# Kernel optimization log

Measured on AMD Instinct MI355X. Metric: run time of the kernel, lower is better.

## Reference

```python
import jax, jax.numpy as jnp
import numpy as np

B, S, D, H, HD = 4, 2048, 1024, 16, 64


def setup_inputs() -> dict:
    key = jax.random.key(0)
    k1, k2, k3 = jax.random.split(key, 3)
    x = jax.random.normal(k1, (B, S, D), dtype=jnp.float32)
    w_attn = jax.random.normal(k2, (D, 3, H, HD), dtype=jnp.float32) * 0.02
    b_attn = jnp.zeros((3, H, HD), dtype=jnp.float32)
    w_proj = jax.random.normal(k3, (H, HD, D), dtype=jnp.float32) * 0.02
    b_proj = jnp.zeros((D,), dtype=jnp.float32)
    return {"x": x, "w_attn": w_attn, "b_attn": b_attn, "w_proj": w_proj, "b_proj": b_proj}


def reference(x, w_attn, b_attn, w_proj, b_proj):
    # c_attn: [B,S,D] x [D,3,H,HD] -> [B,3,H,S,HD]
    qkv = jnp.einsum('bsd,dqhe->bqhse', x, w_attn) + b_attn[None, :, :, None, :]
    q, k, v = qkv[:, 0], qkv[:, 1], qkv[:, 2]  # each [B,H,S,HD]
    scale = 1.0 / jnp.sqrt(jnp.asarray(HD, dtype=q.dtype))
    scores = jnp.einsum('bhse,bhte->bhst', q * scale, k)  # [B,H,S,S]
    causal = jnp.tril(jnp.ones((S, S), dtype=bool))
    scores = jnp.where(causal, scores, jnp.asarray(-1e9, dtype=scores.dtype))
    attn = jax.nn.softmax(scores, axis=-1)
    out = jnp.einsum('bhst,bhte->bhse', attn, v)  # [B,H,S,HD]
    # c_proj: contract (heads, head_size) -> embed
    return jnp.einsum('bhse,hed->bsd', out, w_proj) + b_proj
```

## Files before the change

kernel.cpp:

```cpp
#include <hip/hip_runtime.h>

#define NB 4
#define NS 2048
#define ND 1024
#define NH 16
#define NE 64
#define NM (NB*NS)

typedef __attribute__((ext_vector_type(8))) __bf16 bf16x8;
typedef __attribute__((ext_vector_type(8))) unsigned short us8;
typedef __attribute__((ext_vector_type(4))) float f32x4;

__device__ __forceinline__ float bf2f(unsigned short h) {
  union { unsigned u; float f; } c; c.u = ((unsigned)h) << 16; return c.f;
}
__device__ __forceinline__ unsigned short f2bf(float f) {
  union { float f; unsigned u; } c; c.f = f;
  return (unsigned short)((c.u + 0x7fffu + ((c.u >> 16) & 1u)) >> 16);
}
__device__ __forceinline__ void load16_to_lds(const void* g, void* l) {
  __builtin_amdgcn_global_load_lds(
      (__attribute__((address_space(1))) void*)(void*)(unsigned long long)(const char*)g,
      (__attribute__((address_space(3))) void*)l, 16, 0, 0);
}

__global__ void detect_dtype(const unsigned* __restrict__ x, int* __restrict__ flag) {
  __shared__ int cnt;
  if (threadIdx.x == 0) cnt = 0;
  __syncthreads();
  unsigned w = x[((unsigned)threadIdx.x * 16381u) & ((1u << 21) - 1u)];
  unsigned lo = w & 0xFFFFu;
  int e = (int)((lo >> 7) & 0xFF);
  int plausible = (lo == 0u) || (e >= 100 && e <= 142);
  atomicAdd(&cnt, plausible);
  __syncthreads();
  if (threadIdx.x == 0) *flag = (cnt >= 192) ? 1 : 0;
}

__global__ void conv_to_bf16(const void* __restrict__ src, unsigned short* __restrict__ dst,
                             int n, const int* __restrict__ flag) {
  int stride = gridDim.x * blockDim.x;
  int i0 = blockIdx.x * blockDim.x + threadIdx.x;
  if (*flag) {
    const unsigned short* s = (const unsigned short*)src;
    for (int i = i0; i < n; i += stride) dst[i] = s[i];
  } else {
    const float* s = (const float*)src;
    for (int i = i0; i < n; i += stride) dst[i] = f2bf(s[i]);
  }
}

__global__ __launch_bounds__(256) void transpose_conv(const void* __restrict__ in,
                                                      unsigned short* __restrict__ out,
                                                      int K, int N, const int* __restrict__ flag) {
  __shared__ unsigned short tile[32][33];
  int n0 = blockIdx.x * 32, k0 = blockIdx.y * 32;
  int tx = threadIdx.x, ty = threadIdx.y;
  if (*flag) {
    const unsigned short* p = (const unsigned short*)in;
#pragma unroll
    for (int i = 0; i < 4; ++i)
      tile[ty + 8*i][tx] = p[(size_t)(k0 + ty + 8*i) * N + n0 + tx];
  } else {
    const float* p = (const float*)in;
#pragma unroll
    for (int i = 0; i < 4; ++i)
      tile[ty + 8*i][tx] = f2bf(p[(size_t)(k0 + ty + 8*i) * N + n0 + tx]);
  }
  __syncthreads();
#pragma unroll
  for (int i = 0; i < 4; ++i)
    out[(size_t)(n0 + ty + 8*i) * K + k0 + tx] = tile[tx][ty + 8*i];
}

__device__ __forceinline__ void gemm_core(const unsigned short* __restrict__ A,
                                          const unsigned short* __restrict__ Bt,
                                          int K, int m0, int n0,
                                          unsigned short* As, unsigned short* Bs,
                                          f32x4 (&acc)[4][4]) {
  int t = threadIdx.x;
  int lane = t & 63;
  int w = t >> 6, wr = w >> 1, wc = w & 1;
  int frm = lane & 15, fko = (lane >> 4) * 8;
  for (int kk = 0; kk < K; kk += 32) {
#pragma unroll
    for (int c = 0; c < 2; ++c) {
      int L = c * 256 + t;
      int r = L >> 2, ko = (L & 3) * 8;
      load16_to_lds(A  + (size_t)(m0 + r) * K + kk + ko, (char*)As + L * 16);
      load16_to_lds(Bt + (size_t)(n0 + r) * K + kk + ko, (char*)Bs + L * 16);
    }
    __syncthreads();
    bf16x8 a[4], b[4];
#pragma unroll
    for (int i = 0; i < 4; ++i) a[i] = *(const bf16x8*)(As + (64*wr + 16*i + frm) * 32 + fko);
#pragma unroll
    for (int j = 0; j < 4; ++j) b[j] = *(const bf16x8*)(Bs + (64*wc + 16*j + frm) * 32 + fko);
#pragma unroll
    for (int i = 0; i < 4; ++i)
#pragma unroll
      for (int j = 0; j < 4; ++j)
        acc[i][j] = __builtin_amdgcn_mfma_f32_16x16x32_bf16(a[i], b[j], acc[i][j], 0, 0, 0);
    __syncthreads();
  }
}

__global__ __launch_bounds__(256) void gemm_qkv(const unsigned short* __restrict__ X,
                                                const unsigned short* __restrict__ W1T,
                                                const unsigned short* __restrict__ battn,
                                                unsigned short* __restrict__ qb,
                                                unsigned short* __restrict__ kb,
                                                unsigned short* __restrict__ vb) {
  __shared__ unsigned short As[128 * 32];
  __shared__ unsigned short Bs[128 * 32];
  int m0 = blockIdx.y * 128, n0 = blockIdx.x * 128;
  f32x4 acc[4][4] = {};
  gemm_core(X, W1T, ND, m0, n0, As, Bs, acc);
  int t = threadIdx.x, lane = t & 63, w = t >> 6, wr = w >> 1, wc = w & 1;
  int coln = lane & 15, rbase = (lane >> 4) * 4;
#pragma unroll
  for (int j = 0; j < 4; ++j) {
    int nn = n0 + 64*wc + 16*j + coln;
    int qq = nn >> 10;
    int h  = (nn >> 6) & 15;
    int e  = nn & 63;
    float bias = bf2f(battn[nn]);
    unsigned short* dst = (qq == 0) ? qb : ((qq == 1) ? kb : vb);
    float scale = (qq == 0) ? (0.125f * 1.44269504f) : 1.0f;
#pragma unroll
    for (int i = 0; i < 4; ++i) {
#pragma unroll
      for (int rr = 0; rr < 4; ++rr) {
        int mm = m0 + 64*wr + 16*i + rbase + rr;
        int bb = mm >> 11, s = mm & 2047;
        float v = (acc[i][j][rr] + bias) * scale;
        size_t idx;
        if (qq == 2) idx = (((size_t)bb * NH + h) * NE + e) * NS + s;
        else         idx = (((size_t)bb * NH + h) * NS + s) * NE + e;
        dst[idx] = f2bf(v);
      }
    }
  }
}

__global__ __launch_bounds__(256) void attn_causal(const unsigned short* __restrict__ qb,
                                                   const unsigned short* __restrict__ kb,
                                                   const unsigned short* __restrict__ vtb,
                                                   unsigned short* __restrict__ ob) {
  __shared__ unsigned short QPs[128 * 64];
  __shared__ unsigned short Ks[2][64 * 64];
  __shared__ unsigned short Vt[2][64 * 64];

  int t = threadIdx.x, lane = t & 63, w = t >> 6;
  int qd = lane >> 4, li = lane & 15;
  int sw0 = ((qd ^ (li & 7)) * 8);
  int sw1 = (((4 + qd) ^ (li & 7)) * 8);
  int p = blockIdx.x;
  int bh = blockIdx.y;
  size_t base = (size_t)bh * NS * NE;
  int bb = bh >> 4, hh = bh & 15;

  bf16x8 onesf;
#pragma unroll
  for (int j = 0; j < 8; ++j) onesf[j] = (__bf16)1.0f;

  auto stage_kv = [&](int k0, unsigned short* Ksb, unsigned short* Vtb) {
#pragma unroll
    for (int c = 0; c < 2; ++c) {
      int ch = c * 256 + t;
      int r = ch >> 3, jl = (ch & 7) ^ (r & 7);
      load16_to_lds(kb  + base + (size_t)(k0 + r) * NE + jl * 8, (char*)Ksb + ch * 16);
      load16_to_lds(vtb + base + (size_t)r * NS + k0 + jl * 8,   (char*)Vtb + ch * 16);
    }
  };

#pragma unroll 1
  for (int phase = 0; phase < 2; ++phase) {
    int qt = (phase == 0) ? (15 - p) : p;
    int q0 = qt * 128;

    asm volatile("s_waitcnt lgkmcnt(0)\n\ts_barrier" ::: "memory");
#pragma unroll
    for (int c = 0; c < 4; ++c) {
      int ch = c * 256 + t;
      int r = ch >> 3, jl = (ch & 7) ^ (r & 7);
      load16_to_lds(qb + base + (size_t)(q0 + r) * NE + jl * 8, (char*)QPs + ch * 16);
    }
    asm volatile("s_waitcnt vmcnt(0)\n\ts_barrier" ::: "memory");

    bf16x8 qa[2][2];
#pragma unroll
    for (int i = 0; i < 2; ++i) {
      const unsigned short* qr = QPs + (32*w + 16*i + li) * 64;
      qa[i][0] = *(const bf16x8*)(qr + sw0);
      qa[i][1] = *(const bf16x8*)(qr + sw1);
    }

    f32x4 o[2][4] = {};
    float l_run[2][4] = {};

    stage_kv(0, Ks[0], Vt[0]);

    int ktmax = 2 * qt + 1;
    for (int kt = 0; kt <= ktmax; ++kt) {
      int cur = kt & 1;
      asm volatile("s_waitcnt lgkmcnt(0)\n\ts_barrier" ::: "memory");
      if (kt < ktmax) {
        stage_kv((kt + 1) * 64, Ks[cur ^ 1], Vt[cur ^ 1]);
        asm volatile("s_waitcnt vmcnt(4)\n\ts_barrier" ::: "memory");
      } else {
        asm volatile("s_waitcnt vmcnt(0)\n\ts_barrier" ::: "memory");
      }

      int k0 = kt * 64;
      const unsigned short* Ksc = Ks[cur];
      const unsigned short* Vtc = Vt[cur];

      bf16x8 kfr[4][2];
#pragma unroll
      for (int c = 0; c < 4; ++c) {
        const unsigned short* kr = Ksc + (16*c + li) * 64;
        kfr[c][0] = *(const bf16x8*)(kr + sw0);
        kfr[c][1] = *(const bf16x8*)(kr + sw1);
      }

      int need_mask = (kt >= 2 * qt);
#pragma unroll
      for (int i = 0; i < 2; ++i) {
        f32x4 sfr[4];
#pragma unroll
        for (int c = 0; c < 4; ++c) {
          f32x4 s = {};
          s = __builtin_amdgcn_mfma_f32_16x16x32_bf16(qa[i][0], kfr[c][0], s, 0, 0, 0);
          s = __builtin_amdgcn_mfma_f32_16x16x32_bf16(qa[i][1], kfr[c][1], s, 0, 0, 0);
          sfr[c] = s;
        }
#pragma unroll
        for (int c = 0; c < 4; ++c) {
#pragma unroll
          for (int rr = 0; rr < 4; ++rr) {
            float sv = fminf(fmaxf(sfr[c][rr], -60.f), 60.f);
            float pv = exp2f(sv);
            if (need_mask) {
              int colk = k0 + 16*c + li;
              int rowq = q0 + 32*w + 16*i + qd*4 + rr;
              if (colk > rowq) pv = 0.f;
            }
            int prow = 32*w + 16*i + qd*4 + rr;
            int lo = 2*c + (li >> 3);
            QPs[prow * 64 + ((lo ^ (prow & 7)) * 8) + (li & 7)] =
                (unsigned short)(__float_as_uint(pv) >> 16);
          }
        }
      }

      bf16x8 pa[2][2];
#pragma unroll
      for (int i = 0; i < 2; ++i) {
        const unsigned short* pr = QPs + (32*w + 16*i + li) * 64;
        pa[i][0] = *(const bf16x8*)(pr + sw0);
        pa[i][1] = *(const bf16x8*)(pr + sw1);
      }

#pragma unroll
      for (int i = 0; i < 2; ++i) {
        f32x4 sm = {};
        sm = __builtin_amdgcn_mfma_f32_16x16x32_bf16(pa[i][0], onesf, sm, 0, 0, 0);
        sm = __builtin_amdgcn_mfma_f32_16x16x32_bf16(pa[i][1], onesf, sm, 0, 0, 0);
#pragma unroll
        for (int rr = 0; rr < 4; ++rr) l_run[i][rr] += sm[rr];
      }

#pragma unroll
      for (int c = 0; c < 4; ++c) {
        const unsigned short* vr = Vtc + (16*c + li) * 64;
        bf16x8 vf0 = *(const bf16x8*)(vr + sw0);
        bf16x8 vf1 = *(const bf16x8*)(vr + sw1);
#pragma unroll
        for (int i = 0; i < 2; ++i) {
          o[i][c] = __builtin_amdgcn_mfma_f32_16x16x32_bf16(pa[i][0], vf0, o[i][c], 0, 0, 0);
          o[i][c] = __builtin_amdgcn_mfma_f32_16x16x32_bf16(pa[i][1], vf1, o[i][c], 0, 0, 0);
        }
      }
    }

#pragma unroll
    for (int i = 0; i < 2; ++i)
#pragma unroll
      for (int c = 0; c < 4; ++c)
#pragma unroll
        for (int rr = 0; rr < 4; ++rr) {
          int rowm = 32*w + 16*i + qd*4 + rr;
          float inv = 1.0f / fmaxf(l_run[i][rr], 1e-30f);
          float ov = o[i][c][rr] * inv;
          int e = 16*c + li;
          ob[(((size_t)bb * NS + (q0 + rowm)) * NH + hh) * NE + e] = f2bf(ov);
        }
  }
}

__global__ __launch_bounds__(256) void gemm_proj(const unsigned short* __restrict__ A,
                                                 const unsigned short* __restrict__ W2T,
                                                 const unsigned short* __restrict__ bproj,
                                                 void* __restrict__ outv,
                                                 const int* __restrict__ flag) {
  __shared__ unsigned short As[128 * 32];
  __shared__ unsigned short Bs[128 * 32];
  int m0 = blockIdx.y * 128, n0 = blockIdx.x * 128;
  f32x4 acc[4][4] = {};
  gemm_core(A, W2T, ND, m0, n0, As, Bs, acc);
  int isbf = *flag;
  unsigned short* out16 = (unsigned short*)outv;
  float* out32 = (float*)outv;
  int t = threadIdx.x, lane = t & 63, w = t >> 6, wr = w >> 1, wc = w & 1;
  int coln = lane & 15, rbase = (lane >> 4) * 4;
#pragma unroll
  for (int j = 0; j < 4; ++j) {
    int nn = n0 + 64*wc + 16*j + coln;
    float bias = bf2f(bproj[nn]);
#pragma unroll
    for (int i = 0; i < 4; ++i) {
#pragma unroll
      for (int rr = 0; rr < 4; ++rr) {
        int mm = m0 + 64*wr + 16*i + rbase + rr;
        float v = acc[i][j][rr] + bias;
        if (isbf) out16[(size_t)mm * ND + nn] = f2bf(v);
        else      out32[(size_t)mm * ND + nn] = v;
      }
    }
  }
}

extern "C" void kernel_launch(void* const* d_in, const int* in_sizes, int n_in,
                              void* d_out, int out_size, void* d_ws, size_t ws_size,
                              hipStream_t stream) {
  (void)in_sizes; (void)n_in; (void)out_size; (void)ws_size;
  char* ws = (char*)d_ws;
  unsigned short* W1T = (unsigned short*)(ws);
  unsigned short* W2T = (unsigned short*)(ws + 6291456);
  unsigned short* qb  = (unsigned short*)(ws + 8388608);
  unsigned short* kb  = (unsigned short*)(ws + 25165824);
  unsigned short* vb  = (unsigned short*)(ws + 41943040);
  unsigned short* ob  = (unsigned short*)(ws + 58720256);
  unsigned short* bac = (unsigned short*)(ws + 75497472);
  unsigned short* bpc = (unsigned short*)(ws + 75505664);
  int*            flg = (int*)(ws + 75513856);
  unsigned short* xc  = ob;

  detect_dtype<<<1, 256, 0, stream>>>((const unsigned*)d_in[0], flg);
  conv_to_bf16<<<2048, 256, 0, stream>>>(d_in[0], xc,  NB*NS*ND, flg);
  conv_to_bf16<<<12,   256, 0, stream>>>(d_in[2], bac, 3*NH*NE, flg);
  conv_to_bf16<<<4,    256, 0, stream>>>(d_in[4], bpc, ND, flg);

  transpose_conv<<<dim3(3072/32, 1024/32), dim3(32, 8), 0, stream>>>(d_in[1], W1T, 1024, 3072, flg);
  transpose_conv<<<dim3(1024/32, 1024/32), dim3(32, 8), 0, stream>>>(d_in[3], W2T, 1024, 1024, flg);
  gemm_qkv<<<dim3(3072/128, NM/128), 256, 0, stream>>>(xc, W1T, bac, qb, kb, vb);
  attn_causal<<<dim3(8, 64), 256, 0, stream>>>(qb, kb, vb, ob);
  gemm_proj<<<dim3(1024/128, NM/128), 256, 0, stream>>>(ob, W2T, bpc, d_out, flg);
}
```

Baseline: 310.3 us.

## Split attention into one query tile per block with 32-key tiles

The causal attention kernel no longer pairs two query tiles per block. It launches 1024 blocks, one per (batch-head, query tile), and orders them through a lookup table so heavy and light tiles interleave. Key/value tiles shrink from 64 to 32 keys, and the kernel gets a min-blocks-per-SM launch bound of 4, to cut LDS and register use and raise occupancy. The score clamp before exp2 is removed. The costs are more per-tile barriers, more block launches, and possible overflow of exp2 without the clamp.

New measurement: 300.1 us. 3.3% less time.

```diff
diff --git a/kernel.cpp b/kernel.cpp
--- a/kernel.cpp
+++ b/kernel.cpp
@@ -8,7 +8,6 @@
 #define NM (NB*NS)
 
 typedef __attribute__((ext_vector_type(8))) __bf16 bf16x8;
-typedef __attribute__((ext_vector_type(8))) unsigned short us8;
 typedef __attribute__((ext_vector_type(4))) float f32x4;
 
 __device__ __forceinline__ float bf2f(unsigned short h) {
@@ -143,20 +142,25 @@
   }
 }
 
-__global__ __launch_bounds__(256) void attn_causal(const unsigned short* __restrict__ qb,
-                                                   const unsigned short* __restrict__ kb,
-                                                   const unsigned short* __restrict__ vtb,
-                                                   unsigned short* __restrict__ ob) {
+__global__ __launch_bounds__(256, 4) void attn_causal(const unsigned short* __restrict__ qb,
+                                                      const unsigned short* __restrict__ kb,
+                                                      const unsigned short* __restrict__ vtb,
+                                                      unsigned short* __restrict__ ob) {
   __shared__ unsigned short QPs[128 * 64];
-  __shared__ unsigned short Ks[2][64 * 64];
-  __shared__ unsigned short Vt[2][64 * 64];
+  __shared__ unsigned short Ks[2][32 * 64];
+  __shared__ unsigned short Vt[2][32 * 64];
 
   int t = threadIdx.x, lane = t & 63, w = t >> 6;
   int qd = lane >> 4, li = lane & 15;
   int sw0 = ((qd ^ (li & 7)) * 8);
   int sw1 = (((4 + qd) ^ (li & 7)) * 8);
-  int p = blockIdx.x;
-  int bh = blockIdx.y;
+
+  const int qtab[4][4] = {{15,8,7,0},{14,9,6,1},{13,10,5,2},{12,11,4,3}};
+  int bi = blockIdx.x;
+  int bh = bi & 63;
+  int qt = qtab[(bi >> 6) & 3][bi >> 8];
+  int q0 = qt * 128;
+  int NT = 4 * qt + 4;
   size_t base = (size_t)bh * NS * NE;
   int bb = bh >> 4, hh = bh & 15;
 
@@ -164,139 +168,115 @@
 #pragma unroll
   for (int j = 0; j < 8; ++j) onesf[j] = (__bf16)1.0f;
 
-  auto stage_kv = [&](int k0, unsigned short* Ksb, unsigned short* Vtb) {
+  auto stage_kv = [&](int kt, int buf) {
+    int k0 = kt * 32;
+    int r = t >> 3, p = t & 7, l = p ^ (r & 7);
+    load16_to_lds(kb + base + (size_t)(k0 + r) * NE + l * 8, (char*)Ks[buf] + t * 16);
+    int e = 2 * r + (l >> 2);
+    load16_to_lds(vtb + base + (size_t)e * NS + k0 + (l & 3) * 8, (char*)Vt[buf] + t * 16);
+  };
+
+#pragma unroll
+  for (int c = 0; c < 4; ++c) {
+    int ch = c * 256 + t;
+    int r = ch >> 3, jl = (ch & 7) ^ (r & 7);
+    load16_to_lds(qb + base + (size_t)(q0 + r) * NE + jl * 8, (char*)QPs + ch * 16);
+  }
+  stage_kv(0, 0);
+  asm volatile("s_waitcnt vmcnt(2)\n\ts_barrier" ::: "memory");
+
+  bf16x8 qa[2][2];
+#pragma unroll
+  for (int i = 0; i < 2; ++i) {
+    const unsigned short* qr = QPs + (32*w + 16*i + li) * 64;
+    qa[i][0] = *(const bf16x8*)(qr + sw0);
+    qa[i][1] = *(const bf16x8*)(qr + sw1);
+  }
+
+  f32x4 o[2][4] = {};
+  float l_run[2][4] = {};
+
+  for (int kt = 0; kt < NT; ++kt) {
+    int cur = kt & 1;
+    asm volatile("s_waitcnt lgkmcnt(0)\n\ts_barrier" ::: "memory");
+    if (kt + 1 < NT) {
+      stage_kv(kt + 1, cur ^ 1);
+      asm volatile("s_waitcnt vmcnt(2)\n\ts_barrier" ::: "memory");
+    } else {
+      asm volatile("s_waitcnt vmcnt(0)\n\ts_barrier" ::: "memory");
+    }
+
+    int k0 = kt * 32;
+    const unsigned short* Ksc = Ks[cur];
+    const unsigned short* Vtc = Vt[cur];
+
+    bf16x8 kfr[2][2];
 #pragma unroll
     for (int c = 0; c < 2; ++c) {
-      int ch = c * 256 + t;
-      int r = ch >> 3, jl = (ch & 7) ^ (r & 7);
-      load16_to_lds(kb  + base + (size_t)(k0 + r) * NE + jl * 8, (char*)Ksb + ch * 16);
-      load16_to_lds(vtb + base + (size_t)r * NS + k0 + jl * 8,   (char*)Vtb + ch * 16);
-    }
-  };
-
-#pragma unroll 1
-  for (int phase = 0; phase < 2; ++phase) {
-    int qt = (phase == 0) ? (15 - p) : p;
-    int q0 = qt * 128;
-
-    asm volatile("s_waitcnt lgkmcnt(0)\n\ts_barrier" ::: "memory");
-#pragma unroll
-    for (int c = 0; c < 4; ++c) {
-      int ch = c * 256 + t;
-      int r = ch >> 3, jl = (ch & 7) ^ (r & 7);
-      load16_to_lds(qb + base + (size_t)(q0 + r) * NE + jl * 8, (char*)QPs + ch * 16);
-    }
-    asm volatile("s_waitcnt vmcnt(0)\n\ts_barrier" ::: "memory");
-
-    bf16x8 qa[2][2];
+      const unsigned short* kr = Ksc + (16*c + li) * 64;
+      kfr[c][0] = *(const bf16x8*)(kr + sw0);
+      kfr[c][1] = *(const bf16x8*)(kr + sw1);
+    }
+
+    int need_mask = (k0 >= q0);
 #pragma unroll
     for (int i = 0; i < 2; ++i) {
-      const unsigned short* qr = QPs + (32*w + 16*i + li) * 64;
-      qa[i][0] = *(const bf16x8*)(qr + sw0);
-      qa[i][1] = *(const bf16x8*)(qr + sw1);
-    }
-
-    f32x4 o[2][4] = {};
-    float l_run[2][4] = {};
-
-    stage_kv(0, Ks[0], Vt[0]);
-
-    int ktmax = 2 * qt + 1;
-    for (int kt = 0; kt <= ktmax; ++kt) {
-      int cur = kt & 1;
-      asm volatile("s_waitcnt lgkmcnt(0)\n\ts_barrier" ::: "memory");
-      if (kt < ktmax) {
-        stage_kv((kt + 1) * 64, Ks[cur ^ 1], Vt[cur ^ 1]);
-        asm volatile("s_waitcnt vmcnt(4)\n\ts_barrier" ::: "memory");
-      } else {
-        asm volatile("s_waitcnt vmcnt(0)\n\ts_barrier" ::: "memory");
-      }
-
-      int k0 = kt * 64;
-      const unsigned short* Ksc = Ks[cur];
-      const unsigned short* Vtc = Vt[cur];
-
-      bf16x8 kfr[4][2];
-#pragma unroll
-      for (int c = 0; c < 4; ++c) {
-        const unsigned short* kr = Ksc + (16*c + li) * 64;
-        kfr[c][0] = *(const bf16x8*)(kr + sw0);
-        kfr[c][1] = *(const bf16x8*)(kr + sw1);
-      }
-
-      int need_mask = (kt >= 2 * qt);
-#pragma unroll
-      for (int i = 0; i < 2; ++i) {
-        f32x4 sfr[4];
-#pragma unroll
-        for (int c = 0; c < 4; ++c) {
-          f32x4 s = {};
-          s = __builtin_amdgcn_mfma_f32_16x16x32_bf16(qa[i][0], kfr[c][0], s, 0, 0, 0);
-          s = __builtin_amdgcn_mfma_f32_16x16x32_bf16(qa[i][1], kfr[c][1], s, 0, 0, 0);
-          sfr[c] = s;
-        }
-#pragma unroll
-        for (int c = 0; c < 4; ++c) {
-#pragma unroll
-          for (int rr = 0; rr < 4; ++rr) {
-            float sv = fminf(fmaxf(sfr[c][rr], -60.f), 60.f);
-            float pv = exp2f(sv);
-            if (need_mask) {
-              int colk = k0 + 16*c + li;
-              int rowq = q0 + 32*w + 16*i + qd*4 + rr;
-              if (colk > rowq) pv = 0.f;
-            }
-            int prow = 32*w + 16*i + qd*4 + rr;
-            int lo = 2*c + (li >> 3);
-            QPs[prow * 64 + ((lo ^ (prow & 7)) * 8) + (li & 7)] =
-                (unsigned short)(__float_as_uint(pv) >> 16);
+#pragma unroll
+      for (int c = 0; c < 2; ++c) {
+        f32x4 s = {};
+        s = __builtin_amdgcn_mfma_f32_16x16x32_bf16(qa[i][0], kfr[c][0], s, 0, 0, 0);
+        s = __builtin_amdgcn_mfma_f32_16x16x32_bf16(qa[i][1], kfr[c][1], s, 0, 0, 0);
+#pragma unroll
+        for (int rr = 0; rr < 4; ++rr) {
+          float pv = exp2f(s[rr]);
+          if (need_mask) {
+            int colk = k0 + 16*c + li;
+            int rowq = q0 + 32*w + 16*i + qd*4 + rr;
+            if (colk > rowq) pv = 0.f;
           }
+          int prow = 32*w + 16*i + qd*4 + rr;
+          int lo = 2*c + (li >> 3);
+          QPs[prow * 64 + ((lo ^ (prow & 7)) * 8) + (li & 7)] =
+              (unsigned short)(__float_as_uint(pv) >> 16);
         }
       }
-
-      bf16x8 pa[2][2];
-#pragma unroll
-      for (int i = 0; i < 2; ++i) {
-        const unsigned short* pr = QPs + (32*w + 16*i + li) * 64;
-        pa[i][0] = *(const bf16x8*)(pr + sw0);
-        pa[i][1] = *(const bf16x8*)(pr + sw1);
+    }
+
+    bf16x8 pa[2];
+#pragma unroll
+    for (int i = 0; i < 2; ++i)
+      pa[i] = *(const bf16x8*)(QPs + (32*w + 16*i + li) * 64 + sw0);
+
+#pragma unroll
+    for (int i = 0; i < 2; ++i) {
+      f32x4 sm = {};
+      sm = __builtin_amdgcn_mfma_f32_16x16x32_bf16(pa[i], onesf, sm, 0, 0, 0);
+#pragma unroll
+      for (int rr = 0; rr < 4; ++rr) l_run[i][rr] += sm[rr];
+    }
+
+#pragma unroll
+    for (int c2 = 0; c2 < 4; ++c2) {
+      const unsigned short* vr = Vtc + (8*c2 + (li >> 1)) * 64;
+      bf16x8 vf = *(const bf16x8*)(vr + ((((li & 1) * 4 + qd) ^ ((li >> 1) & 7)) * 8));
+#pragma unroll
+      for (int i = 0; i < 2; ++i)
+        o[i][c2] = __builtin_amdgcn_mfma_f32_16x16x32_bf16(pa[i], vf, o[i][c2], 0, 0, 0);
+    }
+  }
+
+#pragma unroll
+  for (int i = 0; i < 2; ++i)
+#pragma unroll
+    for (int c = 0; c < 4; ++c)
+#pragma unroll
+      for (int rr = 0; rr < 4; ++rr) {
+        int rowm = 32*w + 16*i + qd*4 + rr;
+        float inv = 1.0f / fmaxf(l_run[i][rr], 1e-30f);
+        float ov = o[i][c][rr] * inv;
+        int e = 16*c + li;
+        ob[(((size_t)bb * NS + (q0 + rowm)) * NH + hh) * NE + e] = f2bf(ov);
       }
-
-#pragma unroll
-      for (int i = 0; i < 2; ++i) {
-        f32x4 sm = {};
-        sm = __builtin_amdgcn_mfma_f32_16x16x32_bf16(pa[i][0], onesf, sm, 0, 0, 0);
-        sm = __builtin_amdgcn_mfma_f32_16x16x32_bf16(pa[i][1], onesf, sm, 0, 0, 0);
-#pragma unroll
-        for (int rr = 0; rr < 4; ++rr) l_run[i][rr] += sm[rr];
-      }
-
-#pragma unroll
-      for (int c = 0; c < 4; ++c) {
-        const unsigned short* vr = Vtc + (16*c + li) * 64;
-        bf16x8 vf0 = *(const bf16x8*)(vr + sw0);
-        bf16x8 vf1 = *(const bf16x8*)(vr + sw1);
-#pragma unroll
-        for (int i = 0; i < 2; ++i) {
-          o[i][c] = __builtin_amdgcn_mfma_f32_16x16x32_bf16(pa[i][0], vf0, o[i][c], 0, 0, 0);
-          o[i][c] = __builtin_amdgcn_mfma_f32_16x16x32_bf16(pa[i][1], vf1, o[i][c], 0, 0, 0);
-        }
-      }
-    }
-
-#pragma unroll
-    for (int i = 0; i < 2; ++i)
-#pragma unroll
-      for (int c = 0; c < 4; ++c)
-#pragma unroll
-        for (int rr = 0; rr < 4; ++rr) {
-          int rowm = 32*w + 16*i + qd*4 + rr;
-          float inv = 1.0f / fmaxf(l_run[i][rr], 1e-30f);
-          float ov = o[i][c][rr] * inv;
-          int e = 16*c + li;
-          ob[(((size_t)bb * NS + (q0 + rowm)) * NH + hh) * NE + e] = f2bf(ov);
-        }
-  }
 }
 
 __global__ __launch_bounds__(256) void gemm_proj(const unsigned short* __restrict__ A,
@@ -355,6 +335,6 @@
   transpose_conv<<<dim3(3072/32, 1024/32), dim3(32, 8), 0, stream>>>(d_in[1], W1T, 1024, 3072, flg);
   transpose_conv<<<dim3(1024/32, 1024/32), dim3(32, 8), 0, stream>>>(d_in[3], W2T, 1024, 1024, flg);
   gemm_qkv<<<dim3(3072/128, NM/128), 256, 0, stream>>>(xc, W1T, bac, qb, kb, vb);
-  attn_causal<<<dim3(8, 64), 256, 0, stream>>>(qb, kb, vb, ob);
+  attn_causal<<<dim3(1024), 256, 0, stream>>>(qb, kb, vb, ob);
   gemm_proj<<<dim3(1024/128, NM/128), 256, 0, stream>>>(ob, W2T, bpc, d_out, flg);
 }
```
